# Performance work log

Hardware: AMD Instinct MI355X
Metric: run time of the kernel (lower is better)

The kernel has to match this reference:

```python
import jax, jax.numpy as jnp
import numpy as np

EPS = 1e-5
K = 20
H = [64, 64, 128, 256]

def knn_idx(x, k):
    # x: [B,N,3] -> idx [B,N,k] of nearest neighbors by squared euclidean distance
    inner = -2.0 * jnp.einsum('bnc,bmc->bnm', x, x)
    x2 = jnp.sum(x * x, axis=-1)                      # [B,N]
    neg_d = -x2[:, :, None] - inner - x2[:, None, :]  # -||xi-xj||^2
    _, idx = jax.lax.top_k(neg_d, k)
    return idx

def edge_features(x, idx):
    # x: [B,N,C], idx: [B,N,k] -> [B,N,k,2C] = concat(neighbor - center, center)
    nbr = jax.vmap(lambda xb, ib: xb[ib])(x, idx)     # [B,N,k,C]
    ctr = jnp.broadcast_to(x[:, :, None, :], nbr.shape)
    return jnp.concatenate([nbr - ctr, ctr], axis=-1)

def edge_conv(e, W, b, g, be):
    # e: [B,N,k,Cin]; 1x1 Conv2d == einsum; BatchNorm2d (batch stats) + LeakyReLU(0.2)
    h = jnp.einsum('bnkc,oc->bnko', e, W) + b
    m = jnp.mean(h, axis=(0, 1, 2))
    v = jnp.var(h, axis=(0, 1, 2))
    h = g * (h - m) / jnp.sqrt(v + EPS) + be
    h = jnp.where(h >= 0, h, 0.2 * h)
    return jnp.max(h, axis=2)                          # max over k -> [B,N,O]

def setup_inputs() -> dict:
    key = jax.random.key(0)
    ks = jax.random.split(key, 32)
    B, N = 8, 2048
    d = {"x": jax.random.normal(ks[0], (B, N, 3), dtype=jnp.float32)}
    ins = [2 * 3, 2 * H[0], 2 * H[1], 2 * H[2]]
    for i in range(4):
        o, c = H[i], ins[i]
        d[f"W{i}"] = jax.random.normal(ks[1 + 4 * i], (o, c), dtype=jnp.float32) / np.sqrt(c)
        d[f"b{i}"] = jnp.zeros((o,), dtype=jnp.float32)
        d[f"g{i}"] = jnp.ones((o,), dtype=jnp.float32)
        d[f"be{i}"] = jnp.zeros((o,), dtype=jnp.float32)
    cin, cout = sum(H), 2 * 512
    d["Wf"] = jax.random.normal(ks[20], (cout, cin), dtype=jnp.float32) / np.sqrt(cin)
    d["bf"] = jnp.zeros((cout,), dtype=jnp.float32)
    return d

def reference(x, W0, b0, g0, be0, W1, b1, g1, be1, W2, b2, g2, be2, W3, b3, g3, be3, Wf, bf):
    params = [(W0, b0, g0, be0), (W1, b1, g1, be1), (W2, b2, g2, be2), (W3, b3, g3, be3)]
    xs = []
    h = x  # [B,N,C]
    for (W, b, g, be) in params:
        idx = knn_idx(h if h.shape[-1] != 3 else h, K) if h.shape[-1] == 3 else knn_idx(h, K)
        e = edge_features(h, idx)
        h = edge_conv(e, W, b, g, be)
        xs.append(h)
    xcat = jnp.concatenate(xs, axis=-1)               # [B,N,512]
    out = jnp.einsum('bnc,oc->bno', xcat, Wf) + bf    # 1x1 Conv1d
    return jnp.max(out, axis=1)                        # global max pool -> [B,1024]
```

## Files before the change

### kernel.cpp

```cpp
#include <hip/hip_runtime.h>
#include <cstdint>
#include <cstddef>


constexpr int NB = 8;
constexpr int NP = 2048;
constexpr int KK = 20;

typedef short bf16x8 __attribute__((ext_vector_type(8)));
typedef float f32x16 __attribute__((ext_vector_type(16)));

__device__ __forceinline__ f32x16 MF(bf16x8 a, bf16x8 b, f32x16 c) {
  return __builtin_amdgcn_mfma_f32_32x32x16_bf16(a, b, c, 0, 0, 0);
}
__device__ __forceinline__ unsigned short bfh(float f) {
  return (unsigned short)(__float_as_uint(f) >> 16);
}
__device__ __forceinline__ float bff(unsigned short u) {
  return __uint_as_float(((unsigned)u) << 16);
}
__device__ __forceinline__ void split2(float v, unsigned short& h, unsigned short& l) {
  h = bfh(v); l = bfh(v - bff(h));
}

#define FMA16(AV, BV, ACC)                                          \
  {                                                                 \
    const float _a[4] = {AV.x, AV.y, AV.z, AV.w};                   \
    const float _b[4] = {BV.x, BV.y, BV.z, BV.w};                   \
    _Pragma("unroll")                                               \
    for (int _e = 0; _e < 4; ++_e) {                                \
      _Pragma("unroll")                                             \
      for (int _f = 0; _f < 4; ++_f)                                \
        ACC[_e][_f] = fmaf(_a[_e], _b[_f], ACC[_e][_f]);            \
    }                                                               \
  }

__global__ __launch_bounds__(256) void pad_norms(const float* __restrict__ x,
    float* __restrict__ x4, float* __restrict__ nrm) {
  const int p = blockIdx.x * 256 + threadIdx.x;
  float4 v;
  v.x = x[p * 3 + 0]; v.y = x[p * 3 + 1]; v.z = x[p * 3 + 2]; v.w = 0.f;
  *reinterpret_cast<float4*>(x4 + (size_t)p * 4) = v;
  nrm[p] = v.x * v.x + v.y * v.y + v.z * v.z;
}

__global__ __launch_bounds__(256) void wsplit_all(const float* __restrict__ W1,
    const float* __restrict__ W2, const float* __restrict__ W3,
    const float* __restrict__ Wf,
    unsigned short* __restrict__ wb1, unsigned short* __restrict__ wb2,
    unsigned short* __restrict__ wb3,
    unsigned short* __restrict__ wfh, unsigned short* __restrict__ wfl) {
  const int id = blockIdx.x * 256 + threadIdx.x;
  if (id < 524288) {
    const int row = id >> 9, c = id & 511;
    unsigned short h, l;
    split2(Wf[id], h, l);
    const size_t a = ((((size_t)(row >> 6)) * 64 + (c >> 3)) * 64 + (row & 63)) * 8 + (c & 7);
    wfh[a] = h; wfl[a] = l;
    return;
  }
  int id2 = id - 524288;
  const float* W; unsigned short* wb; int O, C;
  if (id2 < 4096)      { W = W1; wb = wb1; O = 64;  C = 64;  }
  else if (id2 < 12288){ W = W2; wb = wb2; O = 128; C = 64;  id2 -= 4096; }
  else                 { W = W3; wb = wb3; O = 256; C = 128; id2 -= 12288; }
  const int o = id2 / C, c = id2 % C;
  const int K8 = C >> 3;
  const float w1 = W[o * 2 * C + c];
  const float w2 = W[o * 2 * C + C + c];
  unsigned short h, l;
  const int r1 = o, rd = O + o;
  const size_t a1 = (((size_t)(r1 >> 6) * K8 + (c >> 3)) * 64 + (r1 & 63)) * 8 + (c & 7);
  const size_t ad = (((size_t)(rd >> 6) * K8 + (c >> 3)) * 64 + (rd & 63)) * 8 + (c & 7);
  split2(w1, h, l);
  wb[a1] = h; wb[2 * O * C + a1] = l;
  split2(w2 - w1, h, l);
  wb[ad] = h; wb[2 * O * C + ad] = l;
}

__global__ __launch_bounds__(256) void dist0_kernel(const float* __restrict__ X4,
    const float* __restrict__ norms, float* __restrict__ negd, int bbase) {
  __shared__ float sb[640];
  const int t = threadIdx.x, tr = t & 15, tcq = t >> 4;
  const int z = blockIdx.z, b = bbase + z;
  const int i0 = blockIdx.x * 64, j0 = blockIdx.y * 64;
  const int c4 = t >> 6, row = t & 63;
  if (t < 64) sb[512 + t] = norms[b * NP + i0 + t];
  else if (t < 128) sb[512 + t] = norms[b * NP + j0 + (t - 64)];
  sb[c4 * 64 + row] = X4[(size_t)(b * NP + i0 + row) * 4 + c4];
  sb[256 + c4 * 64 + row] = X4[(size_t)(b * NP + j0 + row) * 4 + c4];
  __syncthreads();
  float acc[4][4] = {};
#pragma unroll
  for (int c = 0; c < 4; ++c) {
    const float4 a = *reinterpret_cast<const float4*>(sb + c * 64 + tr * 4);
    const float4 bb = *reinterpret_cast<const float4*>(sb + 256 + c * 64 + tcq * 4);
    FMA16(a, bb, acc);
  }
#pragma unroll
  for (int e = 0; e < 4; ++e) {
    const int rowi = tr * 4 + e;
    const float ni = sb[512 + rowi];
    float4 nd;
    nd.x = 2.f * acc[e][0] - ni - sb[576 + tcq * 4 + 0];
    nd.y = 2.f * acc[e][1] - ni - sb[576 + tcq * 4 + 1];
    nd.z = 2.f * acc[e][2] - ni - sb[576 + tcq * 4 + 2];
    nd.w = 2.f * acc[e][3] - ni - sb[576 + tcq * 4 + 3];
    *reinterpret_cast<float4*>(negd + ((size_t)z * NP + i0 + rowi) * NP + j0 + tcq * 4) = nd;
  }
}

template<int C, int JT, bool HOLD>
__global__ __launch_bounds__(256) void dist_mfma(const unsigned short* __restrict__ xh,
    const unsigned short* __restrict__ xl, int colbase,
    const float* __restrict__ norms, float* __restrict__ negd, int bbase) {
  constexpr int H = C / 16;
  const int t = threadIdx.x, lane = t & 63, w = t >> 6;
  const int half = lane >> 5, l31 = lane & 31;
  const int rt = (w >> 1) * 32, tc = (w & 1) * 32;
  const int z = blockIdx.z, b = bbase + z;
  const int i0 = blockIdx.x * 64;
  const int ti = (b * NP + i0) >> 6;
  const int k8b = colbase >> 3;
  const int col = tc + l31;

  bf16x8 AH[HOLD ? H : 1], AL[HOLD ? H : 1];
  if constexpr (HOLD) {
#pragma unroll
    for (int ch = 0; ch < H; ++ch) {
      const size_t a = (((size_t)ti * 64 + k8b + ch * 2 + half) * 64 + rt + l31) * 8;
      AH[ch] = *reinterpret_cast<const bf16x8*>(xh + a);
      AL[ch] = *reinterpret_cast<const bf16x8*>(xl + a);
    }
  }
  float ni[16];
#pragma unroll
  for (int i = 0; i < 16; ++i) {
    const int row = rt + (i & 3) + 8 * (i >> 2) + 4 * half;
    ni[i] = norms[b * NP + i0 + row];
  }

  for (int jt = 0; jt < JT; ++jt) {
    const int j0 = (blockIdx.y * JT + jt) * 64;
    const int tj = (b * NP + j0) >> 6;
    bf16x8 BH[H], BL[H];
#pragma unroll
    for (int ch = 0; ch < H; ++ch) {
      const size_t a = (((size_t)tj * 64 + k8b + ch * 2 + half) * 64 + col) * 8;
      BH[ch] = *reinterpret_cast<const bf16x8*>(xh + a);
      BL[ch] = *reinterpret_cast<const bf16x8*>(xl + a);
    }
    const float nj = norms[b * NP + j0 + col];

    f32x16 acc;
#pragma unroll
    for (int i = 0; i < 16; ++i) acc[i] = 0.f;
#pragma unroll
    for (int ch = 0; ch < H; ++ch) {
      bf16x8 ah, al;
      if constexpr (HOLD) {
        ah = AH[ch]; al = AL[ch];
      } else {
        const size_t a = (((size_t)ti * 64 + k8b + ch * 2 + half) * 64 + rt + l31) * 8;
        ah = *reinterpret_cast<const bf16x8*>(xh + a);
        al = *reinterpret_cast<const bf16x8*>(xl + a);
      }
      acc = MF(ah, BH[ch], acc); acc = MF(ah, BL[ch], acc); acc = MF(al, BH[ch], acc);
    }
#pragma unroll
    for (int i = 0; i < 16; ++i) {
      const int row = rt + (i & 3) + 8 * (i >> 2) + 4 * half;
      negd[((size_t)z * NP + i0 + row) * NP + j0 + col] = 2.f * acc[i] - ni[i] - nj;
    }
  }
}

__global__ __launch_bounds__(256) void knn_select_kernel(const float* __restrict__ negd,
    int* __restrict__ idxout, int bbase) {
  __shared__ float sb[4 * 2112];
  const int t = threadIdx.x, lane = t & 63, w = t >> 6;
  const int rloc = blockIdx.x * 4 + w;
  const float* rowp = negd + (size_t)rloc * NP;
  float* ws = sb + w * 2112;

#pragma unroll
  for (int m = 0; m < 8; ++m) {
    const int c = m * 256 + lane * 4;
    const float4 d = *reinterpret_cast<const float4*>(rowp + c);
    const int lo = c >> 5, e = c & 31;
    ws[lo * 33 + e + 0] = d.x;
    ws[lo * 33 + e + 1] = d.y;
    ws[lo * 33 + e + 2] = d.z;
    ws[lo * 33 + e + 3] = d.w;
  }
  float v[32];
#pragma unroll
  for (int e = 0; e < 32; ++e) v[e] = ws[lane * 33 + e];

  float lm = v[0]; int lp = 0;
#pragma unroll
  for (int e = 1; e < 32; ++e)
    if (v[e] > lm) { lm = v[e]; lp = e; }

  int* op = idxout + (size_t)(bbase * NP + rloc) * KK;
  for (int r = 0; r < KK; ++r) {
    float wm = lm;
#pragma unroll
    for (int o = 1; o < 64; o <<= 1) wm = fmaxf(wm, __shfl_xor(wm, o));
    const unsigned long long bal = __ballot(lm == wm);
    const int wl = __ffsll(bal) - 1;
    if (lane == wl) {
      op[r] = lane * 32 + lp;
#pragma unroll
      for (int e = 0; e < 32; ++e)
        if (e == lp) v[e] = -__builtin_inff();
      lm = v[0]; lp = 0;
#pragma unroll
      for (int e = 1; e < 32; ++e)
        if (v[e] > lm) { lm = v[e]; lp = e; }
    }
  }
}

__global__ __launch_bounds__(256) void pt_gemm0(const float* __restrict__ x,
    const float* __restrict__ W, const float* __restrict__ bias,
    float* __restrict__ Y, float* __restrict__ T) {
  const int t = threadIdx.x;
  const int o = t & 63;
  const int g = blockIdx.x * 4 + (t >> 6);
  const float x0 = x[(size_t)g * 3 + 0], x1 = x[(size_t)g * 3 + 1], x2 = x[(size_t)g * 3 + 2];
  const float w10 = W[o * 6 + 0], w11 = W[o * 6 + 1], w12 = W[o * 6 + 2];
  const float w20 = W[o * 6 + 3], w21 = W[o * 6 + 4], w22 = W[o * 6 + 5];
  Y[(size_t)g * 64 + o] = w10 * x0 + w11 * x1 + w12 * x2;
  T[(size_t)g * 64 + o] = (w20 - w10) * x0 + (w21 - w11) * x1 + (w22 - w12) * x2 + bias[o];
}

template<int C, int O2>
__global__ __launch_bounds__(256) void pt_gemm(const unsigned short* __restrict__ xh,
    const unsigned short* __restrict__ xl, int colbase,
    const unsigned short* __restrict__ wch, const unsigned short* __restrict__ wcl,
    const float* __restrict__ bias, float* __restrict__ Y, float* __restrict__ T) {
  constexpr int K8 = C / 8;
  constexpr int H = K8 / 2;
  constexpr int O = O2 / 2;
  const int t = threadIdx.x, lane = t & 63, w = t >> 6;
  const int half = lane >> 5, l31 = lane & 31;
  const int rt = (w >> 1) * 32, tc = (w & 1) * 32;
  const int n0 = blockIdx.x * 64, o0 = blockIdx.y * 64;
  const int tn = n0 >> 6, to = o0 >> 6;
  const int k8b = colbase >> 3;
  const int col = o0 + tc + l31;

  bf16x8 BH[H], BL[H];
#pragma unroll
  for (int ch = 0; ch < H; ++ch) {
    const size_t a = (((size_t)to * K8 + ch * 2 + half) * 64 + tc + l31) * 8;
    BH[ch] = *reinterpret_cast<const bf16x8*>(wch + a);
    BL[ch] = *reinterpret_cast<const bf16x8*>(wcl + a);
  }

  f32x16 acc;
#pragma unroll
  for (int i = 0; i < 16; ++i) acc[i] = 0.f;
#pragma unroll
  for (int ch = 0; ch < H; ++ch) {
    const size_t a = (((size_t)tn * 64 + k8b + ch * 2 + half) * 64 + rt + l31) * 8;
    const bf16x8 ah = *reinterpret_cast<const bf16x8*>(xh + a);
    const bf16x8 al = *reinterpret_cast<const bf16x8*>(xl + a);
    acc = MF(ah, BH[ch], acc); acc = MF(ah, BL[ch], acc); acc = MF(al, BH[ch], acc);
  }

  if (col < O) {
#pragma unroll
    for (int i = 0; i < 16; ++i) {
      const int row = n0 + rt + (i & 3) + 8 * (i >> 2) + 4 * half;
      Y[(size_t)row * O + col] = acc[i];
    }
  } else {
    const float bv = bias[col - O];
#pragma unroll
    for (int i = 0; i < 16; ++i) {
      const int row = n0 + rt + (i & 3) + 8 * (i >> 2) + 4 * half;
      T[(size_t)row * O + (col - O)] = acc[i] + bv;
    }
  }
}

template<int O>
__global__ __launch_bounds__(256) void edge_reduce(const float* __restrict__ Y,
    const float* __restrict__ T, const int* __restrict__ idx,
    float* __restrict__ outmax, float* __restrict__ ssum, float* __restrict__ ssq) {
  constexpr int PTS = 32;
  constexpr int NG = 256 / O;
  const int t = threadIdx.x;
  const int o = t % O, ng = t / O;
  const int g0 = blockIdx.x * PTS;
  float sacc = 0.f, qacc = 0.f;
  for (int p = ng; p < PTS; p += NG) {
    const int g = g0 + p;
    const int b = g >> 11;
    const float tv = T[(size_t)g * O + o];
    const int* ip = idx + (size_t)g * KK;
    int ji[KK];
#pragma unroll
    for (int k = 0; k < KK; ++k) ji[k] = ip[k];
    float vs[KK];
#pragma unroll
    for (int k = 0; k < KK; ++k) vs[k] = Y[(size_t)(b * NP + ji[k]) * O + o];
    float mx = -__builtin_inff();
#pragma unroll
    for (int k = 0; k < KK; ++k) {
      const float h = vs[k] + tv;
      mx = fmaxf(mx, h);
      sacc += h;
      qacc = fmaf(h, h, qacc);
    }
    outmax[(size_t)g * O + o] = mx;
  }
  atomicAdd(ssum + o, sacc);
  atomicAdd(ssq + o, qacc);
}

template<int O, bool WN>
__global__ __launch_bounds__(256) void bnrelu_kernel(const float* __restrict__ fA,
    const float* __restrict__ ssum, const float* __restrict__ ssq,
    const float* __restrict__ g, const float* __restrict__ be,
    unsigned short* __restrict__ xh, unsigned short* __restrict__ xl, int colbase,
    float* __restrict__ nrm) {
  constexpr float INV = 1.0f / 327680.0f;
  constexpr int K8 = O / 8;
  const int id = blockIdx.x * 256 + threadIdx.x;
  const int r = id & 63;
  const int k8loc = (id >> 6) % K8;
  const int tile = (id >> 6) / K8;
  const int n = tile * 64 + r;
  const int c0 = k8loc * 8;

  float hv[8];
  {
    const float4 p0 = *reinterpret_cast<const float4*>(fA + (size_t)n * O + c0);
    const float4 p1 = *reinterpret_cast<const float4*>(fA + (size_t)n * O + c0 + 4);
    hv[0] = p0.x; hv[1] = p0.y; hv[2] = p0.z; hv[3] = p0.w;
    hv[4] = p1.x; hv[5] = p1.y; hv[6] = p1.z; hv[7] = p1.w;
  }
  unsigned short hh[8], ll[8];
  float s = 0.f;
#pragma unroll
  for (int j = 0; j < 8; ++j) {
    const int col = c0 + j;
    const float m = ssum[col] * INV;
    const float v = ssq[col] * INV - m * m;
    const float sc = g[col] / sqrtf(v + 1e-5f);
    float val = (hv[j] - m) * sc + be[col];
    val = (val >= 0.f) ? val : 0.2f * val;
    split2(val, hh[j], ll[j]);
    const float recon = bff(hh[j]) + bff(ll[j]);
    s = fmaf(recon, recon, s);
  }
  const size_t ob = (((size_t)tile * 64 + (colbase >> 3) + k8loc) * 64 + r) * 8;
  uint4 ph, pl;
  ph.x = (unsigned)hh[0] | ((unsigned)hh[1] << 16);
  ph.y = (unsigned)hh[2] | ((unsigned)hh[3] << 16);
  ph.z = (unsigned)hh[4] | ((unsigned)hh[5] << 16);
  ph.w = (unsigned)hh[6] | ((unsigned)hh[7] << 16);
  pl.x = (unsigned)ll[0] | ((unsigned)ll[1] << 16);
  pl.y = (unsigned)ll[2] | ((unsigned)ll[3] << 16);
  pl.z = (unsigned)ll[4] | ((unsigned)ll[5] << 16);
  pl.w = (unsigned)ll[6] | ((unsigned)ll[7] << 16);
  *reinterpret_cast<uint4*>(xh + ob) = ph;
  *reinterpret_cast<uint4*>(xl + ob) = pl;
  if (WN) atomicAdd(nrm + n, s);
}

__global__ __launch_bounds__(256) void final_mfma(const unsigned short* __restrict__ xh,
    const unsigned short* __restrict__ xl, const unsigned short* __restrict__ wfh,
    const unsigned short* __restrict__ wfl, unsigned* __restrict__ outenc) {
  __shared__ float fr[128];
  const int t = threadIdx.x, lane = t & 63, w = t >> 6;
  const int half = lane >> 5, l31 = lane & 31;
  const int rt = (w >> 1) * 32, tc = (w & 1) * 32;
  const int b = blockIdx.z, n0 = blockIdx.x * 128, o0 = blockIdx.y * 64;
  const int tn = (b * NP + n0) >> 6, to = o0 >> 6;

  f32x16 acc0, acc1;
#pragma unroll
  for (int i = 0; i < 16; ++i) { acc0[i] = 0.f; acc1[i] = 0.f; }

  for (int cc = 0; cc < 4; ++cc) {
    bf16x8 BH[8], BL[8];
#pragma unroll
    for (int ch = 0; ch < 8; ++ch) {
      const int k8 = cc * 16 + ch * 2 + half;
      const size_t a = (((size_t)to * 64 + k8) * 64 + tc + l31) * 8;
      BH[ch] = *reinterpret_cast<const bf16x8*>(wfh + a);
      BL[ch] = *reinterpret_cast<const bf16x8*>(wfl + a);
    }
#pragma unroll
    for (int ch = 0; ch < 8; ++ch) {
      const int k8 = cc * 16 + ch * 2 + half;
      const size_t a = (((size_t)tn * 64 + k8) * 64 + rt + l31) * 8;
      const bf16x8 ah = *reinterpret_cast<const bf16x8*>(xh + a);
      const bf16x8 al = *reinterpret_cast<const bf16x8*>(xl + a);
      acc0 = MF(ah, BH[ch], acc0); acc0 = MF(ah, BL[ch], acc0); acc0 = MF(al, BH[ch], acc0);
    }
#pragma unroll
    for (int ch = 0; ch < 8; ++ch) {
      const int k8 = cc * 16 + ch * 2 + half;
      const size_t a = (((size_t)(tn + 1) * 64 + k8) * 64 + rt + l31) * 8;
      const bf16x8 ah = *reinterpret_cast<const bf16x8*>(xh + a);
      const bf16x8 al = *reinterpret_cast<const bf16x8*>(xl + a);
      acc1 = MF(ah, BH[ch], acc1); acc1 = MF(ah, BL[ch], acc1); acc1 = MF(al, BH[ch], acc1);
    }
  }

  float M = fmaxf(acc0[0], acc1[0]);
#pragma unroll
  for (int i = 1; i < 16; ++i) M = fmaxf(M, fmaxf(acc0[i], acc1[i]));
  M = fmaxf(M, __shfl_xor(M, 32));
  fr[w * 32 + l31] = M;
  __syncthreads();
  if (t < 64) {
    const float Mc = fmaxf(fr[t], fr[64 + t]);
    const unsigned ub = __float_as_uint(Mc);
    const unsigned key = (ub & 0x80000000u) ? ~ub : (ub | 0x80000000u);
    atomicMax(outenc + b * 1024 + o0 + t, key);
  }
}

__global__ __launch_bounds__(256) void decode_kernel(const unsigned int* __restrict__ enc,
    const float* __restrict__ bf, float* __restrict__ out) {
  const int gid = blockIdx.x * 256 + threadIdx.x;
  const unsigned key = enc[gid];
  const unsigned ubits = (key & 0x80000000u) ? (key & 0x7fffffffu) : ~key;
  out[gid] = __uint_as_float(ubits) + bf[gid & 1023];
}

extern "C" void kernel_launch(void* const* d_in, const int* in_sizes, int n_in,
                              void* d_out, int out_size, void* d_ws, size_t ws_size,
                              hipStream_t stream) {
  (void)in_sizes; (void)n_in; (void)out_size; (void)ws_size;
  const float* x   = (const float*)d_in[0];
  const float* W0  = (const float*)d_in[1];
  const float* b0  = (const float*)d_in[2];
  const float* g0  = (const float*)d_in[3];
  const float* be0 = (const float*)d_in[4];
  const float* W1  = (const float*)d_in[5];
  const float* b1  = (const float*)d_in[6];
  const float* g1  = (const float*)d_in[7];
  const float* be1 = (const float*)d_in[8];
  const float* W2  = (const float*)d_in[9];
  const float* b2  = (const float*)d_in[10];
  const float* g2  = (const float*)d_in[11];
  const float* be2 = (const float*)d_in[12];
  const float* W3  = (const float*)d_in[13];
  const float* b3  = (const float*)d_in[14];
  const float* g3  = (const float*)d_in[15];
  const float* be3 = (const float*)d_in[16];
  const float* Wf  = (const float*)d_in[17];
  const float* bf  = (const float*)d_in[18];

  float* wsf = (float*)d_ws;
  int* idxb = (int*)d_ws;
  float* stats = wsf + 327680;
  float* nb = wsf + 329728;
  unsigned* outenc = (unsigned*)(wsf + 395264);
  float* x4 = wsf + 403456;
  float* featA = wsf + 468992;
  float* negd = wsf + 4663296;
  float* Yb = negd;
  float* Tb = negd + 4194304;
  unsigned short* xh = (unsigned short*)(wsf + 21440512);
  unsigned short* xl = xh + 8388608;
  unsigned short* wb1 = xl + 8388608;
  unsigned short* wb2 = wb1 + 16384;
  unsigned short* wb3 = wb2 + 32768;
  unsigned short* wfh = wb3 + 131072;
  unsigned short* wfl = wfh + 524288;

  float* normsA = nb, *normsB = nb + 16384, *normsC = nb + 32768, *normsD = nb + 49152;

  hipMemsetAsync(stats, 0, (2048 + 65536) * sizeof(float), stream);
  hipMemsetAsync(outenc, 0, 8192 * sizeof(unsigned), stream);

  const dim3 blk(256, 1, 1);
  const dim3 sgrid(2048, 1, 1);
  const dim3 ergrid(512, 1, 1);

  pad_norms<<<dim3(64), blk, 0, stream>>>(x, x4, normsA);
  wsplit_all<<<dim3(2224), blk, 0, stream>>>(W1, W2, W3, Wf, wb1, wb2, wb3, wfh, wfl);

  for (int cb = 0; cb < 2; ++cb) {
    dist0_kernel<<<dim3(32, 32, 4), blk, 0, stream>>>(x4, normsA, negd, 4 * cb);
    knn_select_kernel<<<sgrid, blk, 0, stream>>>(negd, idxb, 4 * cb);
  }
  pt_gemm0<<<dim3(4096), blk, 0, stream>>>(x, W0, b0, Yb, Tb);
  edge_reduce<64><<<ergrid, blk, 0, stream>>>(Yb, Tb, idxb, featA, stats, stats + 256);
  bnrelu_kernel<64, true><<<dim3(512), blk, 0, stream>>>(featA, stats, stats + 256,
      g0, be0, xh, xl, 0, normsB);

  for (int cb = 0; cb < 2; ++cb) {
    dist_mfma<64, 4, true><<<dim3(32, 8, 4), blk, 0, stream>>>(xh, xl, 0, normsB, negd, 4 * cb);
    knn_select_kernel<<<sgrid, blk, 0, stream>>>(negd, idxb, 4 * cb);
  }
  pt_gemm<64, 128><<<dim3(256, 2), blk, 0, stream>>>(xh, xl, 0, wb1, wb1 + 8192, b1, Yb, Tb);
  edge_reduce<64><<<ergrid, blk, 0, stream>>>(Yb, Tb, idxb, featA, stats + 512, stats + 768);
  bnrelu_kernel<64, true><<<dim3(512), blk, 0, stream>>>(featA, stats + 512, stats + 768,
      g1, be1, xh, xl, 64, normsC);

  for (int cb = 0; cb < 2; ++cb) {
    dist_mfma<64, 4, true><<<dim3(32, 8, 4), blk, 0, stream>>>(xh, xl, 64, normsC, negd, 4 * cb);
    knn_select_kernel<<<sgrid, blk, 0, stream>>>(negd, idxb, 4 * cb);
  }
  pt_gemm<64, 256><<<dim3(256, 4), blk, 0, stream>>>(xh, xl, 64, wb2, wb2 + 16384, b2, Yb, Tb);
  edge_reduce<128><<<ergrid, blk, 0, stream>>>(Yb, Tb, idxb, featA, stats + 1024, stats + 1280);
  bnrelu_kernel<128, true><<<dim3(1024), blk, 0, stream>>>(featA, stats + 1024, stats + 1280,
      g2, be2, xh, xl, 128, normsD);

  for (int cb = 0; cb < 2; ++cb) {
    dist_mfma<128, 2, false><<<dim3(32, 16, 4), blk, 0, stream>>>(xh, xl, 128, normsD, negd, 4 * cb);
    knn_select_kernel<<<sgrid, blk, 0, stream>>>(negd, idxb, 4 * cb);
  }
  pt_gemm<128, 512><<<dim3(256, 8), blk, 0, stream>>>(xh, xl, 128, wb3, wb3 + 65536, b3, Yb, Tb);
  edge_reduce<256><<<ergrid, blk, 0, stream>>>(Yb, Tb, idxb, featA, stats + 1536, stats + 1792);
  bnrelu_kernel<256, false><<<dim3(2048), blk, 0, stream>>>(featA, stats + 1536, stats + 1792,
      g3, be3, xh, xl, 256, nullptr);

  final_mfma<<<dim3(16, 16, 8), blk, 0, stream>>>(xh, xl, wfh, wfl, outenc);
  decode_kernel<<<dim3(32), blk, 0, stream>>>(outenc, bf, (float*)d_out);
}
```

Before: 1.033 ms.

## Fuse MFMA distance computation with streaming top-k selection for kNN layers

For kNN layers 1-3, the full N×N distance matrix is no longer written to global memory and re-read by a separate select kernel. Each block now computes 64x64 distance tiles with MFMA into shared memory and keeps per-thread top-20 lists, pruned by a shared threshold. It writes candidate lists for four column slices, which a small merge kernel reduces to the final indices. The final GEMM also widens its output tile to 128 channels so each loaded activation fragment is reused across two weight tiles. The selection path now has divergent threshold-driven insertion loops, and the fused kernel launches a small grid of 512 blocks per batch half.

```diff
diff --git a/kernel.cpp b/kernel.cpp
--- a/kernel.cpp
+++ b/kernel.cpp
@@ -110,71 +110,6 @@
   }
 }
 
-template<int C, int JT, bool HOLD>
-__global__ __launch_bounds__(256) void dist_mfma(const unsigned short* __restrict__ xh,
-    const unsigned short* __restrict__ xl, int colbase,
-    const float* __restrict__ norms, float* __restrict__ negd, int bbase) {
-  constexpr int H = C / 16;
-  const int t = threadIdx.x, lane = t & 63, w = t >> 6;
-  const int half = lane >> 5, l31 = lane & 31;
-  const int rt = (w >> 1) * 32, tc = (w & 1) * 32;
-  const int z = blockIdx.z, b = bbase + z;
-  const int i0 = blockIdx.x * 64;
-  const int ti = (b * NP + i0) >> 6;
-  const int k8b = colbase >> 3;
-  const int col = tc + l31;
-
-  bf16x8 AH[HOLD ? H : 1], AL[HOLD ? H : 1];
-  if constexpr (HOLD) {
-#pragma unroll
-    for (int ch = 0; ch < H; ++ch) {
-      const size_t a = (((size_t)ti * 64 + k8b + ch * 2 + half) * 64 + rt + l31) * 8;
-      AH[ch] = *reinterpret_cast<const bf16x8*>(xh + a);
-      AL[ch] = *reinterpret_cast<const bf16x8*>(xl + a);
-    }
-  }
-  float ni[16];
-#pragma unroll
-  for (int i = 0; i < 16; ++i) {
-    const int row = rt + (i & 3) + 8 * (i >> 2) + 4 * half;
-    ni[i] = norms[b * NP + i0 + row];
-  }
-
-  for (int jt = 0; jt < JT; ++jt) {
-    const int j0 = (blockIdx.y * JT + jt) * 64;
-    const int tj = (b * NP + j0) >> 6;
-    bf16x8 BH[H], BL[H];
-#pragma unroll
-    for (int ch = 0; ch < H; ++ch) {
-      const size_t a = (((size_t)tj * 64 + k8b + ch * 2 + half) * 64 + col) * 8;
-      BH[ch] = *reinterpret_cast<const bf16x8*>(xh + a);
-      BL[ch] = *reinterpret_cast<const bf16x8*>(xl + a);
-    }
-    const float nj = norms[b * NP + j0 + col];
-
-    f32x16 acc;
-#pragma unroll
-    for (int i = 0; i < 16; ++i) acc[i] = 0.f;
-#pragma unroll
-    for (int ch = 0; ch < H; ++ch) {
-      bf16x8 ah, al;
-      if constexpr (HOLD) {
-        ah = AH[ch]; al = AL[ch];
-      } else {
-        const size_t a = (((size_t)ti * 64 + k8b + ch * 2 + half) * 64 + rt + l31) * 8;
-        ah = *reinterpret_cast<const bf16x8*>(xh + a);
-        al = *reinterpret_cast<const bf16x8*>(xl + a);
-      }
-      acc = MF(ah, BH[ch], acc); acc = MF(ah, BL[ch], acc); acc = MF(al, BH[ch], acc);
-    }
-#pragma unroll
-    for (int i = 0; i < 16; ++i) {
-      const int row = rt + (i & 3) + 8 * (i >> 2) + 4 * half;
-      negd[((size_t)z * NP + i0 + row) * NP + j0 + col] = 2.f * acc[i] - ni[i] - nj;
-    }
-  }
-}
-
 __global__ __launch_bounds__(256) void knn_select_kernel(const float* __restrict__ negd,
     int* __restrict__ idxout, int bbase) {
   __shared__ float sb[4 * 2112];
@@ -220,6 +155,177 @@
         if (v[e] > lm) { lm = v[e]; lp = e; }
     }
   }
+}
+
+template<int C>
+__global__ __launch_bounds__(256) void knn_fused(const unsigned short* __restrict__ xh,
+    const unsigned short* __restrict__ xl, int colbase,
+    const float* __restrict__ norms, float* __restrict__ cval, int* __restrict__ cidx,
+    int bbase) {
+  constexpr int H = C / 16;
+  __shared__ float sd[64 * 68];
+  const int t = threadIdx.x, lane = t & 63, w = t >> 6;
+  const int half = lane >> 5, l31 = lane & 31;
+  const int rt = (w >> 1) * 32, tc = (w & 1) * 32;
+  const int z = blockIdx.z, b = bbase + z;
+  const int i0 = blockIdx.x * 64, js = blockIdx.y;
+  const int ti = (b * NP + i0) >> 6, k8b = colbase >> 3;
+
+  bf16x8 AH[H], AL[H];
+#pragma unroll
+  for (int ch = 0; ch < H; ++ch) {
+    const size_t a = (((size_t)ti * 64 + k8b + ch * 2 + half) * 64 + rt + l31) * 8;
+    AH[ch] = *reinterpret_cast<const bf16x8*>(xh + a);
+    AL[ch] = *reinterpret_cast<const bf16x8*>(xl + a);
+  }
+  float ni[16];
+#pragma unroll
+  for (int i = 0; i < 16; ++i) {
+    const int row = rt + (i & 3) + 8 * (i >> 2) + 4 * half;
+    ni[i] = norms[b * NP + i0 + row];
+  }
+
+  float lv[KK]; int li[KK];
+  float minv = -__builtin_inff(); int minpos = 0;
+  float theta = -__builtin_inff();
+  const int rsel = t >> 2, qsel = t & 3;
+
+  auto ins = [&](float nv, int nj) {
+    if (nv > minv) {
+#pragma unroll
+      for (int e = 0; e < KK; ++e)
+        if (e == minpos) { lv[e] = nv; li[e] = nj; }
+      minv = lv[0]; minpos = 0;
+#pragma unroll
+      for (int e = 1; e < KK; ++e)
+        if (lv[e] < minv) { minv = lv[e]; minpos = e; }
+    }
+  };
+
+  for (int st = 0; st < 8; ++st) {
+    const int j0 = js * 512 + st * 64;
+    const int tj = (b * NP + j0) >> 6;
+
+    f32x16 acc;
+#pragma unroll
+    for (int i = 0; i < 16; ++i) acc[i] = 0.f;
+#pragma unroll
+    for (int ch = 0; ch < H; ++ch) {
+      const size_t a = (((size_t)tj * 64 + k8b + ch * 2 + half) * 64 + tc + l31) * 8;
+      const bf16x8 bh = *reinterpret_cast<const bf16x8*>(xh + a);
+      const bf16x8 bl = *reinterpret_cast<const bf16x8*>(xl + a);
+      acc = MF(AH[ch], bh, acc); acc = MF(AH[ch], bl, acc); acc = MF(AL[ch], bh, acc);
+    }
+    const float nj = norms[b * NP + j0 + tc + l31];
+#pragma unroll
+    for (int i = 0; i < 16; ++i) {
+      const int row = rt + (i & 3) + 8 * (i >> 2) + 4 * half;
+      sd[row * 68 + tc + l31] = 2.f * acc[i] - ni[i] - nj;
+    }
+    __syncthreads();
+
+    const float* rp = sd + rsel * 68 + qsel * 16;
+    const int jb0 = j0 + qsel * 16;
+    if (st == 0) {
+#pragma unroll
+      for (int m = 0; m < 4; ++m) {
+        const float4 dv = *reinterpret_cast<const float4*>(rp + m * 4);
+        const int jb = jb0 + m * 4;
+        lv[m * 4 + 0] = dv.x; li[m * 4 + 0] = jb + 0;
+        lv[m * 4 + 1] = dv.y; li[m * 4 + 1] = jb + 1;
+        lv[m * 4 + 2] = dv.z; li[m * 4 + 2] = jb + 2;
+        lv[m * 4 + 3] = dv.w; li[m * 4 + 3] = jb + 3;
+      }
+    } else if (st == 1) {
+      {
+        const float4 dv = *reinterpret_cast<const float4*>(rp);
+        lv[16] = dv.x; li[16] = jb0 + 0;
+        lv[17] = dv.y; li[17] = jb0 + 1;
+        lv[18] = dv.z; li[18] = jb0 + 2;
+        lv[19] = dv.w; li[19] = jb0 + 3;
+      }
+      minv = lv[0]; minpos = 0;
+#pragma unroll
+      for (int e = 1; e < KK; ++e)
+        if (lv[e] < minv) { minv = lv[e]; minpos = e; }
+#pragma unroll
+      for (int m = 1; m < 4; ++m) {
+        const float4 dv = *reinterpret_cast<const float4*>(rp + m * 4);
+        const int jb = jb0 + m * 4;
+        ins(dv.x, jb + 0); ins(dv.y, jb + 1); ins(dv.z, jb + 2); ins(dv.w, jb + 3);
+      }
+      theta = fmaxf(minv, __shfl_xor(minv, 1));
+      theta = fmaxf(theta, __shfl_xor(theta, 2));
+    } else {
+      unsigned mask = 0;
+#pragma unroll
+      for (int m = 0; m < 4; ++m) {
+        const float4 dv = *reinterpret_cast<const float4*>(rp + m * 4);
+        mask |= (dv.x >= theta ? 1u : 0u) << (m * 4 + 0);
+        mask |= (dv.y >= theta ? 1u : 0u) << (m * 4 + 1);
+        mask |= (dv.z >= theta ? 1u : 0u) << (m * 4 + 2);
+        mask |= (dv.w >= theta ? 1u : 0u) << (m * 4 + 3);
+      }
+      while (__any(mask != 0u)) {
+        if (mask) {
+          const int sB = __ffs(mask) - 1;
+          mask &= mask - 1;
+          ins(rp[sB], jb0 + sB);
+        }
+      }
+      theta = fmaxf(minv, __shfl_xor(minv, 1));
+      theta = fmaxf(theta, __shfl_xor(theta, 2));
+    }
+    __syncthreads();
+  }
+
+  const int base = lane & ~3;
+  for (int sq = 1; sq < 4; ++sq) {
+#pragma unroll
+    for (int e = 0; e < KK; ++e) {
+      const float v = __shfl(lv[e], base + sq);
+      const int j = __shfl(li[e], base + sq);
+      if (qsel == 0) ins(v, j);
+    }
+  }
+  if (qsel == 0) {
+    const size_t rg = (size_t)(b * NP + i0 + rsel);
+    float* vp = cval + (rg * 4 + js) * KK;
+    int* ip = cidx + (rg * 4 + js) * KK;
+#pragma unroll
+    for (int e = 0; e < KK; ++e) { vp[e] = lv[e]; ip[e] = li[e]; }
+  }
+}
+
+__global__ __launch_bounds__(256) void knn_merge_kernel(const float* __restrict__ cval,
+    const int* __restrict__ cidx, int* __restrict__ idxout) {
+  const int r = blockIdx.x * 256 + threadIdx.x;
+  const float* vp = cval + (size_t)r * 80;
+  const int* ip = cidx + (size_t)r * 80;
+  float lv[KK]; int li[KK];
+#pragma unroll
+  for (int e = 0; e < KK; ++e) { lv[e] = vp[e]; li[e] = ip[e]; }
+  float minv = lv[0]; int minpos = 0;
+#pragma unroll
+  for (int e = 1; e < KK; ++e)
+    if (lv[e] < minv) { minv = lv[e]; minpos = e; }
+
+  auto ins = [&](float nv, int nj) {
+    if (nv > minv) {
+#pragma unroll
+      for (int e = 0; e < KK; ++e)
+        if (e == minpos) { lv[e] = nv; li[e] = nj; }
+      minv = lv[0]; minpos = 0;
+#pragma unroll
+      for (int e = 1; e < KK; ++e)
+        if (lv[e] < minv) { minv = lv[e]; minpos = e; }
+    }
+  };
+
+  for (int q = KK; q < 80; ++q) ins(vp[q], ip[q]);
+  int* op = idxout + (size_t)r * KK;
+#pragma unroll
+  for (int e = 0; e < KK; ++e) op[e] = li[e];
 }
 
 __global__ __launch_bounds__(256) void pt_gemm0(const float* __restrict__ x,
@@ -375,55 +481,58 @@
 __global__ __launch_bounds__(256) void final_mfma(const unsigned short* __restrict__ xh,
     const unsigned short* __restrict__ xl, const unsigned short* __restrict__ wfh,
     const unsigned short* __restrict__ wfl, unsigned* __restrict__ outenc) {
-  __shared__ float fr[128];
+  __shared__ float fr[256];
   const int t = threadIdx.x, lane = t & 63, w = t >> 6;
   const int half = lane >> 5, l31 = lane & 31;
   const int rt = (w >> 1) * 32, tc = (w & 1) * 32;
-  const int b = blockIdx.z, n0 = blockIdx.x * 128, o0 = blockIdx.y * 64;
+  const int b = blockIdx.z, n0 = blockIdx.x * 128, o0 = blockIdx.y * 128;
   const int tn = (b * NP + n0) >> 6, to = o0 >> 6;
 
-  f32x16 acc0, acc1;
-#pragma unroll
-  for (int i = 0; i < 16; ++i) { acc0[i] = 0.f; acc1[i] = 0.f; }
+  f32x16 a00, a01, a10, a11;
+#pragma unroll
+  for (int i = 0; i < 16; ++i) { a00[i] = 0.f; a01[i] = 0.f; a10[i] = 0.f; a11[i] = 0.f; }
 
   for (int cc = 0; cc < 4; ++cc) {
-    bf16x8 BH[8], BL[8];
 #pragma unroll
     for (int ch = 0; ch < 8; ++ch) {
       const int k8 = cc * 16 + ch * 2 + half;
-      const size_t a = (((size_t)to * 64 + k8) * 64 + tc + l31) * 8;
-      BH[ch] = *reinterpret_cast<const bf16x8*>(wfh + a);
-      BL[ch] = *reinterpret_cast<const bf16x8*>(wfl + a);
-    }
-#pragma unroll
-    for (int ch = 0; ch < 8; ++ch) {
-      const int k8 = cc * 16 + ch * 2 + half;
-      const size_t a = (((size_t)tn * 64 + k8) * 64 + rt + l31) * 8;
-      const bf16x8 ah = *reinterpret_cast<const bf16x8*>(xh + a);
-      const bf16x8 al = *reinterpret_cast<const bf16x8*>(xl + a);
-      acc0 = MF(ah, BH[ch], acc0); acc0 = MF(ah, BL[ch], acc0); acc0 = MF(al, BH[ch], acc0);
-    }
-#pragma unroll
-    for (int ch = 0; ch < 8; ++ch) {
-      const int k8 = cc * 16 + ch * 2 + half;
-      const size_t a = (((size_t)(tn + 1) * 64 + k8) * 64 + rt + l31) * 8;
-      const bf16x8 ah = *reinterpret_cast<const bf16x8*>(xh + a);
-      const bf16x8 al = *reinterpret_cast<const bf16x8*>(xl + a);
-      acc1 = MF(ah, BH[ch], acc1); acc1 = MF(ah, BL[ch], acc1); acc1 = MF(al, BH[ch], acc1);
-    }
-  }
-
-  float M = fmaxf(acc0[0], acc1[0]);
-#pragma unroll
-  for (int i = 1; i < 16; ++i) M = fmaxf(M, fmaxf(acc0[i], acc1[i]));
-  M = fmaxf(M, __shfl_xor(M, 32));
-  fr[w * 32 + l31] = M;
+      const size_t ab0 = (((size_t)to * 64 + k8) * 64 + tc + l31) * 8;
+      const size_t ab1 = (((size_t)(to + 1) * 64 + k8) * 64 + tc + l31) * 8;
+      const bf16x8 b0h = *reinterpret_cast<const bf16x8*>(wfh + ab0);
+      const bf16x8 b0l = *reinterpret_cast<const bf16x8*>(wfl + ab0);
+      const bf16x8 b1h = *reinterpret_cast<const bf16x8*>(wfh + ab1);
+      const bf16x8 b1l = *reinterpret_cast<const bf16x8*>(wfl + ab1);
+      const size_t aa0 = (((size_t)tn * 64 + k8) * 64 + rt + l31) * 8;
+      const size_t aa1 = (((size_t)(tn + 1) * 64 + k8) * 64 + rt + l31) * 8;
+      const bf16x8 a0h = *reinterpret_cast<const bf16x8*>(xh + aa0);
+      const bf16x8 a0l = *reinterpret_cast<const bf16x8*>(xl + aa0);
+      const bf16x8 a1h = *reinterpret_cast<const bf16x8*>(xh + aa1);
+      const bf16x8 a1l = *reinterpret_cast<const bf16x8*>(xl + aa1);
+      a00 = MF(a0h, b0h, a00); a00 = MF(a0h, b0l, a00); a00 = MF(a0l, b0h, a00);
+      a01 = MF(a0h, b1h, a01); a01 = MF(a0h, b1l, a01); a01 = MF(a0l, b1h, a01);
+      a10 = MF(a1h, b0h, a10); a10 = MF(a1h, b0l, a10); a10 = MF(a1l, b0h, a10);
+      a11 = MF(a1h, b1h, a11); a11 = MF(a1h, b1l, a11); a11 = MF(a1l, b1h, a11);
+    }
+  }
+
+  float M0 = fmaxf(a00[0], a10[0]);
+  float M1 = fmaxf(a01[0], a11[0]);
+#pragma unroll
+  for (int i = 1; i < 16; ++i) {
+    M0 = fmaxf(M0, fmaxf(a00[i], a10[i]));
+    M1 = fmaxf(M1, fmaxf(a01[i], a11[i]));
+  }
+  M0 = fmaxf(M0, __shfl_xor(M0, 32));
+  M1 = fmaxf(M1, __shfl_xor(M1, 32));
+  fr[w * 32 + l31] = M0;
+  fr[128 + w * 32 + l31] = M1;
   __syncthreads();
-  if (t < 64) {
-    const float Mc = fmaxf(fr[t], fr[64 + t]);
+  if (t < 128) {
+    const int ot = t >> 6, cl = t & 63;
+    const float Mc = fmaxf(fr[ot * 128 + cl], fr[ot * 128 + 64 + cl]);
     const unsigned ub = __float_as_uint(Mc);
     const unsigned key = (ub & 0x80000000u) ? ~ub : (ub | 0x80000000u);
-    atomicMax(outenc + b * 1024 + o0 + t, key);
+    atomicMax(outenc + b * 1024 + o0 + ot * 64 + cl, key);
   }
 }
 
@@ -469,6 +578,8 @@
   float* negd = wsf + 4663296;
   float* Yb = negd;
   float* Tb = negd + 4194304;
+  float* cval = negd + 8388608;
+  int* cidx = (int*)(negd + 9699328);
   unsigned short* xh = (unsigned short*)(wsf + 21440512);
   unsigned short* xl = xh + 8388608;
   unsigned short* wb1 = xl + 8388608;
@@ -483,6 +594,7 @@
   hipMemsetAsync(outenc, 0, 8192 * sizeof(unsigned), stream);
 
   const dim3 blk(256, 1, 1);
+  const dim3 fgrid(32, 4, 4);
   const dim3 sgrid(2048, 1, 1);
   const dim3 ergrid(512, 1, 1);
 
@@ -498,33 +610,30 @@
   bnrelu_kernel<64, true><<<dim3(512), blk, 0, stream>>>(featA, stats, stats + 256,
       g0, be0, xh, xl, 0, normsB);
 
-  for (int cb = 0; cb < 2; ++cb) {
-    dist_mfma<64, 4, true><<<dim3(32, 8, 4), blk, 0, stream>>>(xh, xl, 0, normsB, negd, 4 * cb);
-    knn_select_kernel<<<sgrid, blk, 0, stream>>>(negd, idxb, 4 * cb);
-  }
+  knn_fused<64><<<fgrid, blk, 0, stream>>>(xh, xl, 0, normsB, cval, cidx, 0);
+  knn_fused<64><<<fgrid, blk, 0, stream>>>(xh, xl, 0, normsB, cval, cidx, 4);
+  knn_merge_kernel<<<dim3(64), blk, 0, stream>>>(cval, cidx, idxb);
   pt_gemm<64, 128><<<dim3(256, 2), blk, 0, stream>>>(xh, xl, 0, wb1, wb1 + 8192, b1, Yb, Tb);
   edge_reduce<64><<<ergrid, blk, 0, stream>>>(Yb, Tb, idxb, featA, stats + 512, stats + 768);
   bnrelu_kernel<64, true><<<dim3(512), blk, 0, stream>>>(featA, stats + 512, stats + 768,
       g1, be1, xh, xl, 64, normsC);
 
-  for (int cb = 0; cb < 2; ++cb) {
-    dist_mfma<64, 4, true><<<dim3(32, 8, 4), blk, 0, stream>>>(xh, xl, 64, normsC, negd, 4 * cb);
-    knn_select_kernel<<<sgrid, blk, 0, stream>>>(negd, idxb, 4 * cb);
-  }
+  knn_fused<64><<<fgrid, blk, 0, stream>>>(xh, xl, 64, normsC, cval, cidx, 0);
+  knn_fused<64><<<fgrid, blk, 0, stream>>>(xh, xl, 64, normsC, cval, cidx, 4);
+  knn_merge_kernel<<<dim3(64), blk, 0, stream>>>(cval, cidx, idxb);
   pt_gemm<64, 256><<<dim3(256, 4), blk, 0, stream>>>(xh, xl, 64, wb2, wb2 + 16384, b2, Yb, Tb);
   edge_reduce<128><<<ergrid, blk, 0, stream>>>(Yb, Tb, idxb, featA, stats + 1024, stats + 1280);
   bnrelu_kernel<128, true><<<dim3(1024), blk, 0, stream>>>(featA, stats + 1024, stats + 1280,
       g2, be2, xh, xl, 128, normsD);
 
-  for (int cb = 0; cb < 2; ++cb) {
-    dist_mfma<128, 2, false><<<dim3(32, 16, 4), blk, 0, stream>>>(xh, xl, 128, normsD, negd, 4 * cb);
-    knn_select_kernel<<<sgrid, blk, 0, stream>>>(negd, idxb, 4 * cb);
-  }
+  knn_fused<128><<<fgrid, blk, 0, stream>>>(xh, xl, 128, normsD, cval, cidx, 0);
+  knn_fused<128><<<fgrid, blk, 0, stream>>>(xh, xl, 128, normsD, cval, cidx, 4);
+  knn_merge_kernel<<<dim3(64), blk, 0, stream>>>(cval, cidx, idxb);
   pt_gemm<128, 512><<<dim3(256, 8), blk, 0, stream>>>(xh, xl, 128, wb3, wb3 + 65536, b3, Yb, Tb);
   edge_reduce<256><<<ergrid, blk, 0, stream>>>(Yb, Tb, idxb, featA, stats + 1536, stats + 1792);
   bnrelu_kernel<256, false><<<dim3(2048), blk, 0, stream>>>(featA, stats + 1536, stats + 1792,
       g3, be3, xh, xl, 256, nullptr);
 
-  final_mfma<<<dim3(16, 16, 8), blk, 0, stream>>>(xh, xl, wfh, wfl, outenc);
+  final_mfma<<<dim3(16, 8, 8), blk, 0, stream>>>(xh, xl, wfh, wfl, outenc);
   decode_kernel<<<dim3(32), blk, 0, stream>>>(outenc, bf, (float*)d_out);
 }
```

Result: slower. 1.572 ms (+52.2%).
